# Optimization experiments

Hardware: AMD Instinct MI355X
Metric: run time of the kernel (lower is better)

The kernel has to match this reference:

```python
import jax, jax.numpy as jnp
import numpy as np

N = 50000      # nodes
E = 800000     # edges
F_IN = 128     # n_features
H = 4          # n_heads
C1 = 64        # n_hidden (per-head out of layer 1)
C2 = 32        # n_classes (per-head out of layer 2)
NEG_SLOPE = 0.2
EPS = 1e-16


def setup_inputs() -> dict:
    key = jax.random.key(0)
    ks = jax.random.split(key, 12)
    x = jax.random.normal(ks[0], (N, F_IN), dtype=jnp.float32)
    edge_index = jax.random.randint(ks[1], (2, E), 0, N, dtype=jnp.int64)
    # layer 1 params (GATConv: shared lin for src/dst, att_src/att_dst vectors, bias)
    W1 = jax.random.normal(ks[2], (F_IN, H * C1), dtype=jnp.float32) * (1.0 / np.sqrt(F_IN))
    att_src1 = jax.random.normal(ks[3], (H, C1), dtype=jnp.float32) * 0.1
    att_dst1 = jax.random.normal(ks[4], (H, C1), dtype=jnp.float32) * 0.1
    b1 = jnp.zeros((C1,), dtype=jnp.float32)
    # layer 2 params
    W2 = jax.random.normal(ks[5], (C1, H * C2), dtype=jnp.float32) * (1.0 / np.sqrt(C1))
    att_src2 = jax.random.normal(ks[6], (H, C2), dtype=jnp.float32) * 0.1
    att_dst2 = jax.random.normal(ks[7], (H, C2), dtype=jnp.float32) * 0.1
    b2 = jnp.zeros((C2,), dtype=jnp.float32)
    return {"x": x, "edge_index": edge_index,
            "W1": W1, "att_src1": att_src1, "att_dst1": att_dst1, "b1": b1,
            "W2": W2, "att_src2": att_src2, "att_dst2": att_dst2, "b2": b2}


def gat_conv(x, src, dst, W, att_src, att_dst, b, heads, out_ch):
    """PyG GATConv with concat=False (head-averaged output)."""
    n = x.shape[0]
    h = (x @ W).reshape(n, heads, out_ch)                 # [N, H, C]
    a_s = jnp.einsum('nhc,hc->nh', h, att_src)            # [N, H]
    a_d = jnp.einsum('nhc,hc->nh', h, att_dst)            # [N, H]
    e = jax.nn.leaky_relu(a_s[src] + a_d[dst], NEG_SLOPE)  # [E, H]
    # segment softmax over edges grouped by destination node
    m = jax.ops.segment_max(e, dst, num_segments=n)        # [N, H]
    m = jnp.where(jnp.isfinite(m), m, 0.0)
    ex = jnp.exp(e - m[dst])                               # [E, H]
    denom = jax.ops.segment_sum(ex, dst, num_segments=n)   # [N, H]
    alpha = ex / (denom[dst] + EPS)                        # [E, H]
    # scatter-add aggregation of attended source features
    msg = alpha[:, :, None] * h[src]                       # [E, H, C]
    out = jax.ops.segment_sum(msg, dst, num_segments=n)    # [N, H, C]
    return out.mean(axis=1) + b                            # [N, C]


def reference(x, edge_index, W1, att_src1, att_dst1, b1, W2, att_src2, att_dst2, b2):
    src, dst = edge_index[0], edge_index[1]
    h = jax.nn.relu(gat_conv(x, src, dst, W1, att_src1, att_dst1, b1, H, C1))
    # dropout is identity in eval mode
    out = gat_conv(h, src, dst, W2, att_src2, att_dst2, b2, H, C2)
    return out
```

## Files before the change

kernel.cpp:

```cpp
#include <hip/hip_runtime.h>
#include <hip/hip_fp16.h>
#include <cstdint>
#include <cstddef>

#define N_NODES 50000
#define N_EDGES 800000
#define F_IN 128
#define H_HEADS 4
#define C1 64
#define C2 32
#define NEG_SLOPE 0.2f
#define EPS_GAT 1e-16f
#define SLOT_CAP 96
#define FILL_BPG 256
#define NODES_PER_GROUP 6250
#define GEMM1_BLOCKS 782
#define CBASE ((int)0xAAAAAAAAu)

typedef _Float16 half8 __attribute__((ext_vector_type(8)));
typedef float f32x4 __attribute__((ext_vector_type(4)));

template<int K, int M>
__device__ __forceinline__ void wtrans_dev(const float* __restrict__ W,
                                           _Float16* __restrict__ Wt,
                                           _Float16* tile, int bm, int bk) {
    const int m0 = bm * 64, k0 = bk * 64;
    const int t = threadIdx.x;
    const int c = t & 63;
#pragma unroll
    for (int j = 0; j < 16; ++j) {
        int r = (t >> 6) + 4 * j;
        tile[c * 66 + r] = (_Float16)W[(size_t)(k0 + r) * M + m0 + c];
    }
    __syncthreads();
#pragma unroll
    for (int j = 0; j < 16; ++j) {
        int m_l = (t >> 6) + 4 * j;
        Wt[(size_t)(m0 + m_l) * K + k0 + c] = tile[m_l * 66 + c];
    }
}

__global__ __launch_bounds__(256) void wtrans_kernel(
        const float* __restrict__ W1, _Float16* __restrict__ wt1,
        const float* __restrict__ W2, _Float16* __restrict__ wt2) {
    __shared__ _Float16 tile[64 * 66];
    const int b = blockIdx.x;
    if (b < 8) {
        wtrans_dev<F_IN, H_HEADS * C1>(W1, wt1, tile, b & 3, b >> 2);
    } else {
        wtrans_dev<C1, H_HEADS * C2>(W2, wt2, tile, b - 8, 0);
    }
}

__device__ __forceinline__ void fill_dev(
        const int* __restrict__ src, const int* __restrict__ dst,
        int* __restrict__ cursor, unsigned short* __restrict__ slots,
        int fb) {
    const int g = (fb + (GEMM1_BLOCKS & 7)) & 7;
    const int bg = fb >> 3;
    const int dlo = g * NODES_PER_GROUP;
    const int dhi = dlo + NODES_PER_GROUP;
    const int4* dst4 = (const int4*)dst;
    const int4* src4 = (const int4*)src;
    constexpr int NV4 = N_EDGES / 4;
    for (int v = bg * 256 + (int)threadIdx.x; v < NV4; v += FILL_BPG * 256) {
        int4 d4 = dst4[v];
        int4 s4 = src4[v];
        if (d4.x >= dlo && d4.x < dhi) {
            unsigned int p = (unsigned int)(atomicAdd(&cursor[d4.x], 1) - CBASE);
            if (p < SLOT_CAP) slots[(size_t)d4.x * SLOT_CAP + p] = (unsigned short)s4.x;
        }
        if (d4.y >= dlo && d4.y < dhi) {
            unsigned int p = (unsigned int)(atomicAdd(&cursor[d4.y], 1) - CBASE);
            if (p < SLOT_CAP) slots[(size_t)d4.y * SLOT_CAP + p] = (unsigned short)s4.y;
        }
        if (d4.z >= dlo && d4.z < dhi) {
            unsigned int p = (unsigned int)(atomicAdd(&cursor[d4.z], 1) - CBASE);
            if (p < SLOT_CAP) slots[(size_t)d4.z * SLOT_CAP + p] = (unsigned short)s4.z;
        }
        if (d4.w >= dlo && d4.w < dhi) {
            unsigned int p = (unsigned int)(atomicAdd(&cursor[d4.w], 1) - CBASE);
            if (p < SLOT_CAP) slots[(size_t)d4.w * SLOT_CAP + p] = (unsigned short)s4.w;
        }
    }
}

template<int K, int M, int Hn, int C, typename InT>
__device__ __forceinline__ void gemm_att_dev(
        const InT* __restrict__ X, const _Float16* __restrict__ Wt,
        _Float16* __restrict__ Hout,
        const float* __restrict__ atts, const float* __restrict__ attd,
        float* __restrict__ as_, float* __restrict__ ad_, int Nr,
        _Float16* Ah, _Float16* Bt, _Float16* Ht, int row0) {
    constexpr int LDK = K + 8;
    constexpr int NCT = M / 64;
    constexpr int HPB = 64 / C;
    const int t = threadIdx.x;
    const int wv = t >> 6;
    const int lane = t & 63;
    const int quad = lane >> 4;
    const int n16 = lane & 15;

    if constexpr (sizeof(InT) == 4) {
        constexpr int KQ = K / 4;
#pragma unroll
        for (int j = 0; j < (64 * KQ) / 256; ++j) {
            int flat = t + 256 * j;
            int r = flat / KQ, kq = flat % KQ;
            int rg = row0 + r;
            float4 v = make_float4(0.f, 0.f, 0.f, 0.f);
            if (rg < Nr) v = *(const float4*)&X[(size_t)rg * K + 4 * kq];
            _Float16 tmp[4] = {(_Float16)v.x, (_Float16)v.y, (_Float16)v.z, (_Float16)v.w};
            *(uint2*)&Ah[r * LDK + 4 * kq] = *(const uint2*)tmp;
        }
    } else {
        constexpr int KQ = K / 8;
#pragma unroll
        for (int j = 0; j < (64 * KQ) / 256; ++j) {
            int flat = t + 256 * j;
            int r = flat / KQ, kq = flat % KQ;
            int rg = row0 + r;
            uint4 v = make_uint4(0u, 0u, 0u, 0u);
            if (rg < Nr) v = *(const uint4*)&X[(size_t)rg * K + 8 * kq];
            *(uint4*)&Ah[r * LDK + 8 * kq] = v;
        }
    }
    __syncthreads();

    half8 af[K / 32];
    const _Float16* Ap = &Ah[(16 * wv + n16) * LDK + 8 * quad];
#pragma unroll
    for (int ki = 0; ki < K / 32; ++ki) af[ki] = *(const half8*)(Ap + 32 * ki);

    for (int ct = 0; ct < NCT; ++ct) {
        const int col0 = 64 * ct;
        __syncthreads();
        {
            constexpr int KQ8 = K / 8;
#pragma unroll
            for (int j = 0; j < (64 * KQ8) / 256; ++j) {
                int flat = t + 256 * j;
                int c = flat / KQ8, kq = flat % KQ8;
                uint4 v = *(const uint4*)&Wt[(size_t)(col0 + c) * K + 8 * kq];
                *(uint4*)&Bt[c * LDK + 8 * kq] = v;
            }
        }
        __syncthreads();

        f32x4 acc[4];
#pragma unroll
        for (int nf = 0; nf < 4; ++nf) acc[nf] = (f32x4){0.f, 0.f, 0.f, 0.f};
#pragma unroll
        for (int ki = 0; ki < K / 32; ++ki) {
#pragma unroll
            for (int nf = 0; nf < 4; ++nf) {
                half8 bf = *(const half8*)&Bt[(16 * nf + n16) * LDK + 32 * ki + 8 * quad];
                acc[nf] = __builtin_amdgcn_mfma_f32_16x16x32_f16(af[ki], bf, acc[nf], 0, 0, 0);
            }
        }

        float dps[HPB][4], dpd[HPB][4];
#pragma unroll
        for (int u = 0; u < HPB; ++u)
#pragma unroll
            for (int r = 0; r < 4; ++r) { dps[u][r] = 0.f; dpd[u][r] = 0.f; }
#pragma unroll
        for (int nf = 0; nf < 4; ++nf) {
            int gc = col0 + 16 * nf + n16;
            float cs = atts[gc], cd = attd[gc];
#pragma unroll
            for (int r = 0; r < 4; ++r) {
                float av = acc[nf][r];
                dps[(16 * nf) / C][r] += av * cs;
                dpd[(16 * nf) / C][r] += av * cd;
            }
        }
#pragma unroll
        for (int u = 0; u < HPB; ++u)
#pragma unroll
            for (int r = 0; r < 4; ++r) {
                float s = dps[u][r], d = dpd[u][r];
#pragma unroll
                for (int off = 1; off < 16; off <<= 1) {
                    s += __shfl_xor(s, off, 64);
                    d += __shfl_xor(d, off, 64);
                }
                dps[u][r] = s; dpd[u][r] = d;
            }
        if (n16 == 0) {
            const int h0 = col0 / C;
#pragma unroll
            for (int r = 0; r < 4; ++r) {
                int row = row0 + 16 * wv + 4 * quad + r;
                if (row < Nr) {
#pragma unroll
                    for (int u = 0; u < HPB; ++u) {
                        as_[row * Hn + h0 + u] = dps[u][r];
                        ad_[row * Hn + h0 + u] = dpd[u][r];
                    }
                }
            }
        }

#pragma unroll
        for (int nf = 0; nf < 4; ++nf)
#pragma unroll
            for (int r = 0; r < 4; ++r)
                Ht[(16 * wv + 4 * quad + r) * 72 + 16 * nf + n16] = (_Float16)acc[nf][r];
        __syncthreads();
#pragma unroll
        for (int j = 0; j < 2; ++j) {
            int chunk = t + 256 * j;
            int r = chunk >> 3, cc = chunk & 7;
            int row = row0 + r;
            if (row < Nr) {
                uint4 v = *(const uint4*)&Ht[r * 72 + 8 * cc];
                *(uint4*)&Hout[(size_t)row * M + col0 + 8 * cc] = v;
            }
        }
    }
}

__global__ __launch_bounds__(256) void gemm1_fill_kernel(
        const float* __restrict__ x, const _Float16* __restrict__ wt1,
        _Float16* __restrict__ h1,
        const float* __restrict__ atts, const float* __restrict__ attd,
        float* __restrict__ as_, float* __restrict__ ad_,
        const int* __restrict__ src, const int* __restrict__ dst,
        int* __restrict__ cursor, unsigned short* __restrict__ slots) {
    constexpr int LDK = F_IN + 8;
    __shared__ _Float16 Ah[64 * LDK];
    __shared__ _Float16 Bt[64 * LDK];
    __shared__ _Float16 Ht[64 * 72];
    if (blockIdx.x < GEMM1_BLOCKS) {
        gemm_att_dev<F_IN, H_HEADS * C1, H_HEADS, C1, float>(
            x, wt1, h1, atts, attd, as_, ad_, N_NODES,
            Ah, Bt, Ht, blockIdx.x * 64);
    } else {
        fill_dev(src, dst, cursor, slots, blockIdx.x - GEMM1_BLOCKS);
    }
}

__global__ __launch_bounds__(256) void agg1_mv_kernel(
        const int* __restrict__ degp, const unsigned short* __restrict__ slots,
        const float* __restrict__ as_, const float* __restrict__ ad_,
        const _Float16* __restrict__ Hm, const float* __restrict__ bias,
        const _Float16* __restrict__ wt2,
        const float* __restrict__ atts2, const float* __restrict__ attd2,
        _Float16* __restrict__ h2, float* __restrict__ as2_,
        float* __restrict__ ad2_, int Nr) {
    constexpr int Hn = H_HEADS;
    constexpr int HC = Hn * C1;
    constexpr int PER = 16;
    int node = blockIdx.x * 4 + (threadIdx.x >> 6);
    int lane = threadIdx.x & 63;
    if (node >= Nr) return;
    const int g = lane >> 4;
    const int l = lane & 15;
    const int h = l >> 2;
    const float ad_h = ad_[node * Hn + h];

    const int dn = min(degp[node] - CBASE, SLOT_CAP);
    const int begin = node * SLOT_CAP;
    const int end = begin + dn;
    const int iters = (dn + 3) >> 2;

    float acc[PER];
#pragma unroll
    for (int t = 0; t < PER; ++t) acc[t] = 0.f;
    float wsum = 0.f;

    int idx = begin + g;
    bool okA = idx < end;
    int sA = (int)slots[okA ? idx : begin];
    float aA = as_[sA * Hn + h];
    uint4 uA[2];
    {
        const uint4* hp = (const uint4*)(Hm + (size_t)sA * HC + l * PER);
        uA[0] = hp[0]; uA[1] = hp[1];
    }

#pragma unroll 2
    for (int it = 0; it < iters; ++it) {
        const int j = idx + 4;
        const bool okB = j < end;
        int sB = (int)slots[okB ? j : begin];
        float aB = as_[sB * Hn + h];
        uint4 uB[2];
        {
            const uint4* hp = (const uint4*)(Hm + (size_t)sB * HC + l * PER);
            uB[0] = hp[0]; uB[1] = hp[1];
        }

        float logit = aA + ad_h;
        float lr = fmaxf(logit, NEG_SLOPE * logit);
        float w = okA ? __expf(lr) : 0.f;
        wsum += w;
#pragma unroll
        for (int v = 0; v < 2; ++v) {
            half8 hv = __builtin_bit_cast(half8, uA[v]);
#pragma unroll
            for (int e = 0; e < 8; ++e)
                acc[8 * v + e] = fmaf((float)hv[e], w, acc[8 * v + e]);
        }
        okA = okB; aA = aB; uA[0] = uB[0]; uA[1] = uB[1];
        idx = j;
    }

#pragma unroll
    for (int t = 0; t < PER; ++t) {
        acc[t] += __shfl_xor(acc[t], 16, 64);
        acc[t] += __shfl_xor(acc[t], 32, 64);
    }
    wsum += __shfl_xor(wsum, 16, 64);
    wsum += __shfl_xor(wsum, 32, 64);
    const float inv = 1.f / (wsum + EPS_GAT);
    const int q = lane & 3;
    float val[PER];
#pragma unroll
    for (int t = 0; t < PER; ++t) {
        float v = acc[t] * inv;
        v += __shfl_xor(v, 4, 64);
        v += __shfl_xor(v, 8, 64);
        v = v * (1.0f / Hn) + bias[q * PER + t];
        val[t] = fmaxf(v, 0.f);
    }

    const int r = lane >> 2;
    float p[8];
#pragma unroll
    for (int k = 0; k < 8; ++k) {
        const _Float16* wrow = wt2 + (size_t)(r + 16 * k) * C1 + q * PER;
        half8 wa = *(const half8*)wrow;
        half8 wb = *(const half8*)(wrow + 8);
        float s = 0.f;
#pragma unroll
        for (int e = 0; e < 8; ++e) s = fmaf((float)wa[e], val[e], s);
#pragma unroll
        for (int e = 0; e < 8; ++e) s = fmaf((float)wb[e], val[8 + e], s);
        p[k] = s;
    }
#pragma unroll
    for (int k = 0; k < 8; ++k) {
        p[k] += __shfl_xor(p[k], 1, 64);
        p[k] += __shfl_xor(p[k], 2, 64);
    }

    float asum[4], adsum[4];
#pragma unroll
    for (int hh = 0; hh < 4; ++hh) {
        int m0 = r + 32 * hh, m1 = m0 + 16;
        float a = p[2 * hh] * atts2[m0] + p[2 * hh + 1] * atts2[m1];
        float d = p[2 * hh] * attd2[m0] + p[2 * hh + 1] * attd2[m1];
        asum[hh] = (q == 0) ? a : 0.f;
        adsum[hh] = (q == 0) ? d : 0.f;
    }
#pragma unroll
    for (int hh = 0; hh < 4; ++hh) {
#pragma unroll
        for (int off = 1; off < 64; off <<= 1) {
            asum[hh] += __shfl_xor(asum[hh], off, 64);
            adsum[hh] += __shfl_xor(adsum[hh], off, 64);
        }
    }
    if (lane == 0) {
#pragma unroll
        for (int hh = 0; hh < 4; ++hh) {
            as2_[node * Hn + hh] = asum[hh];
            ad2_[node * Hn + hh] = adsum[hh];
        }
    }

    if (q == 0) {
        _Float16* hp = h2 + (size_t)node * (H_HEADS * C2);
#pragma unroll
        for (int k = 0; k < 8; ++k) hp[r + 16 * k] = (_Float16)p[k];
    }
}

template<int Hn, int C, bool RELU, bool OUT_F16>
__global__ __launch_bounds__(256) void gat_agg_kernel(
        const int* __restrict__ degp, const unsigned short* __restrict__ slots,
        const float* __restrict__ as_, const float* __restrict__ ad_,
        const _Float16* __restrict__ Hm, const float* __restrict__ bias,
        void* __restrict__ outv, int Nr) {
    constexpr int HC = Hn * C;
    constexpr int PER = HC / 16;
    constexpr int NV = PER / 8;
    int node = blockIdx.x * 4 + (threadIdx.x >> 6);
    int lane = threadIdx.x & 63;
    if (node >= Nr) return;
    const int g = lane >> 4;
    const int l = lane & 15;
    const int h = l >> 2;
    const float ad_h = ad_[node * Hn + h];

    const int dn = min(degp[node] - CBASE, SLOT_CAP);
    const int begin = node * SLOT_CAP;
    const int end = begin + dn;
    const int iters = (dn + 3) >> 2;

    float acc[PER];
#pragma unroll
    for (int t = 0; t < PER; ++t) acc[t] = 0.f;
    float wsum = 0.f;

    int idx = begin + g;
    bool okA = idx < end;
    int sA = (int)slots[okA ? idx : begin];
    float aA = as_[sA * Hn + h];
    uint4 uA[NV];
    {
        const uint4* hp = (const uint4*)(Hm + (size_t)sA * HC + l * PER);
        uA[0] = hp[0];
        if constexpr (NV == 2) uA[1] = hp[1];
    }

#pragma unroll 2
    for (int it = 0; it < iters; ++it) {
        const int j = idx + 4;
        const bool okB = j < end;
        int sB = (int)slots[okB ? j : begin];
        float aB = as_[sB * Hn + h];
        uint4 uB[NV];
        {
            const uint4* hp = (const uint4*)(Hm + (size_t)sB * HC + l * PER);
            uB[0] = hp[0];
            if constexpr (NV == 2) uB[1] = hp[1];
        }

        float logit = aA + ad_h;
        float lr = fmaxf(logit, NEG_SLOPE * logit);
        float w = okA ? __expf(lr) : 0.f;
        wsum += w;
#pragma unroll
        for (int v = 0; v < NV; ++v) {
            half8 hv = __builtin_bit_cast(half8, uA[v]);
#pragma unroll
            for (int e = 0; e < 8; ++e)
                acc[8 * v + e] = fmaf((float)hv[e], w, acc[8 * v + e]);
        }
        okA = okB; aA = aB;
        uA[0] = uB[0];
        if constexpr (NV == 2) uA[1] = uB[1];
        idx = j;
    }

#pragma unroll
    for (int t = 0; t < PER; ++t) {
        acc[t] += __shfl_xor(acc[t], 16, 64);
        acc[t] += __shfl_xor(acc[t], 32, 64);
    }
    wsum += __shfl_xor(wsum, 16, 64);
    wsum += __shfl_xor(wsum, 32, 64);
    const float inv = 1.f / (wsum + EPS_GAT);
    float val[PER];
#pragma unroll
    for (int t = 0; t < PER; ++t) {
        float v = acc[t] * inv;
        v += __shfl_xor(v, 4, 64);
        v += __shfl_xor(v, 8, 64);
        val[t] = v * (1.0f / Hn);
    }
    if (lane < 4) {
        const int c0 = lane * PER;
#pragma unroll
        for (int t = 0; t < PER; ++t) {
            float v = val[t] + bias[c0 + t];
            if (RELU) v = fmaxf(v, 0.f);
            val[t] = v;
        }
        if constexpr (OUT_F16) {
            _Float16* o = (_Float16*)outv;
            _Float16 tmp[PER];
#pragma unroll
            for (int t = 0; t < PER; ++t) tmp[t] = (_Float16)val[t];
            uint4* d4 = (uint4*)&o[(size_t)node * C + c0];
            d4[0] = *(const uint4*)&tmp[0];
            if constexpr (NV == 2) d4[1] = *(const uint4*)&tmp[8];
        } else {
            float* o = (float*)outv;
#pragma unroll
            for (int t4 = 0; t4 < PER / 4; ++t4)
                *(float4*)&o[(size_t)node * C + c0 + 4 * t4] =
                    make_float4(val[4 * t4 + 0], val[4 * t4 + 1],
                                val[4 * t4 + 2], val[4 * t4 + 3]);
        }
    }
}

extern "C" void kernel_launch(void* const* d_in, const int* in_sizes, int n_in,
                              void* d_out, int out_size, void* d_ws, size_t ws_size,
                              hipStream_t stream) {
    const float* x    = (const float*)d_in[0];
    const int*   ei   = (const int*)d_in[1];
    const float* W1   = (const float*)d_in[2];
    const float* as1w = (const float*)d_in[3];
    const float* ad1w = (const float*)d_in[4];
    const float* b1   = (const float*)d_in[5];
    const float* W2   = (const float*)d_in[6];
    const float* as2w = (const float*)d_in[7];
    const float* ad2w = (const float*)d_in[8];
    const float* b2   = (const float*)d_in[9];
    float* out = (float*)d_out;

    const int* src = ei;
    const int* dst = ei + N_EDGES;

    char* ws = (char*)d_ws;
    size_t off = 0;
    auto alloc = [&](size_t bytes) -> void* {
        void* p = ws + off;
        off = (off + bytes + 255) & ~(size_t)255;
        return p;
    };
    int*   cursor = (int*)alloc((size_t)N_NODES * 4);
    float* as1_ = (float*)alloc((size_t)N_NODES * H_HEADS * 4);
    float* ad1_ = (float*)alloc((size_t)N_NODES * H_HEADS * 4);
    float* as2_ = (float*)alloc((size_t)N_NODES * H_HEADS * 4);
    float* ad2_ = (float*)alloc((size_t)N_NODES * H_HEADS * 4);
    _Float16* h1   = (_Float16*)alloc((size_t)N_NODES * H_HEADS * C1 * 2);
    _Float16* h2   = (_Float16*)alloc((size_t)N_NODES * H_HEADS * C2 * 2);
    _Float16* wt1  = (_Float16*)alloc((size_t)(H_HEADS * C1) * F_IN * 2);
    _Float16* wt2  = (_Float16*)alloc((size_t)(H_HEADS * C2) * C1 * 2);
    unsigned short* slots = (unsigned short*)alloc((size_t)N_NODES * SLOT_CAP * 2);

    wtrans_kernel<<<10, 256, 0, stream>>>(W1, wt1, W2, wt2);

    gemm1_fill_kernel<<<GEMM1_BLOCKS + 8 * FILL_BPG, 256, 0, stream>>>(
        x, wt1, h1, as1w, ad1w, as1_, ad1_, src, dst, cursor, slots);

    agg1_mv_kernel<<<(N_NODES + 3) / 4, 256, 0, stream>>>(
        cursor, slots, as1_, ad1_, h1, b1, wt2, as2w, ad2w,
        h2, as2_, ad2_, N_NODES);

    gat_agg_kernel<H_HEADS, C2, false, false><<<(N_NODES + 3) / 4, 256, 0, stream>>>(
        cursor, slots, as2_, ad2_, h2, b2, (void*)out, N_NODES);
}
```

Baseline: 262.4 us.

## Reorder layer-2 linear transform after aggregation and fold attention vectors into W2

Attention logits for layer 2 are now computed from the 64-wide layer-1 output through precomputed vectors W2·att, which an extra wtrans block builds. Layer 1 no longer runs the per-node GEMV. The second aggregation gathers the 64-wide fp16 out1 rows instead of the 128-wide h2 rows and applies W2 per head after the weighted sum, using shared memory and a small matvec per node. This halves the per-edge gather bytes in layer 2 and removes the mid-pipeline GEMV, in exchange for a per-node GEMV after aggregation and some shared-memory traffic.

Measured after the change: 337.4 us. 28.6% more time.

```diff
diff --git a/kernel.cpp b/kernel.cpp
--- a/kernel.cpp
+++ b/kernel.cpp
@@ -18,6 +18,7 @@
 #define CBASE ((int)0xAAAAAAAAu)
 
 typedef _Float16 half8 __attribute__((ext_vector_type(8)));
+typedef _Float16 half4 __attribute__((ext_vector_type(4)));
 typedef float f32x4 __attribute__((ext_vector_type(4)));
 
 template<int K, int M>
@@ -42,13 +43,27 @@
 
 __global__ __launch_bounds__(256) void wtrans_kernel(
         const float* __restrict__ W1, _Float16* __restrict__ wt1,
-        const float* __restrict__ W2, _Float16* __restrict__ wt2) {
+        const float* __restrict__ W2, _Float16* __restrict__ wt2,
+        const float* __restrict__ as2w, const float* __restrict__ ad2w,
+        float* __restrict__ vs2, float* __restrict__ vd2) {
     __shared__ _Float16 tile[64 * 66];
     const int b = blockIdx.x;
     if (b < 8) {
         wtrans_dev<F_IN, H_HEADS * C1>(W1, wt1, tile, b & 3, b >> 2);
+    } else if (b < 10) {
+        wtrans_dev<C1, H_HEADS * C2>(W2, wt2, tile, b - 8, 0);
     } else {
-        wtrans_dev<C1, H_HEADS * C2>(W2, wt2, tile, b - 8, 0);
+        const int t = threadIdx.x;
+        const int h = t >> 6, c = t & 63;
+        float s = 0.f, d = 0.f;
+#pragma unroll
+        for (int c2 = 0; c2 < C2; ++c2) {
+            float w = W2[(size_t)c * (H_HEADS * C2) + h * C2 + c2];
+            s = fmaf(w, as2w[h * C2 + c2], s);
+            d = fmaf(w, ad2w[h * C2 + c2], d);
+        }
+        vs2[h * 64 + c] = s;
+        vd2[h * 64 + c] = d;
     }
 }
 
@@ -241,20 +256,18 @@
     }
 }
 
-__global__ __launch_bounds__(256) void agg1_mv_kernel(
+__global__ __launch_bounds__(256) void agg1_kernel(
         const int* __restrict__ degp, const unsigned short* __restrict__ slots,
         const float* __restrict__ as_, const float* __restrict__ ad_,
         const _Float16* __restrict__ Hm, const float* __restrict__ bias,
-        const _Float16* __restrict__ wt2,
-        const float* __restrict__ atts2, const float* __restrict__ attd2,
-        _Float16* __restrict__ h2, float* __restrict__ as2_,
-        float* __restrict__ ad2_, int Nr) {
+        _Float16* __restrict__ out1,
+        const float* __restrict__ vs2, const float* __restrict__ vd2,
+        float* __restrict__ as2_, float* __restrict__ ad2_) {
     constexpr int Hn = H_HEADS;
     constexpr int HC = Hn * C1;
     constexpr int PER = 16;
     int node = blockIdx.x * 4 + (threadIdx.x >> 6);
     int lane = threadIdx.x & 63;
-    if (node >= Nr) return;
     const int g = lane >> 4;
     const int l = lane & 15;
     const int h = l >> 2;
@@ -315,177 +328,176 @@
     wsum += __shfl_xor(wsum, 16, 64);
     wsum += __shfl_xor(wsum, 32, 64);
     const float inv = 1.f / (wsum + EPS_GAT);
-    const int q = lane & 3;
     float val[PER];
 #pragma unroll
     for (int t = 0; t < PER; ++t) {
         float v = acc[t] * inv;
         v += __shfl_xor(v, 4, 64);
         v += __shfl_xor(v, 8, 64);
-        v = v * (1.0f / Hn) + bias[q * PER + t];
-        val[t] = fmaxf(v, 0.f);
-    }
-
-    const int r = lane >> 2;
-    float p[8];
-#pragma unroll
-    for (int k = 0; k < 8; ++k) {
-        const _Float16* wrow = wt2 + (size_t)(r + 16 * k) * C1 + q * PER;
-        half8 wa = *(const half8*)wrow;
-        half8 wb = *(const half8*)(wrow + 8);
-        float s = 0.f;
-#pragma unroll
-        for (int e = 0; e < 8; ++e) s = fmaf((float)wa[e], val[e], s);
-#pragma unroll
-        for (int e = 0; e < 8; ++e) s = fmaf((float)wb[e], val[8 + e], s);
-        p[k] = s;
-    }
-#pragma unroll
-    for (int k = 0; k < 8; ++k) {
-        p[k] += __shfl_xor(p[k], 1, 64);
-        p[k] += __shfl_xor(p[k], 2, 64);
-    }
-
-    float asum[4], adsum[4];
-#pragma unroll
-    for (int hh = 0; hh < 4; ++hh) {
-        int m0 = r + 32 * hh, m1 = m0 + 16;
-        float a = p[2 * hh] * atts2[m0] + p[2 * hh + 1] * atts2[m1];
-        float d = p[2 * hh] * attd2[m0] + p[2 * hh + 1] * attd2[m1];
-        asum[hh] = (q == 0) ? a : 0.f;
-        adsum[hh] = (q == 0) ? d : 0.f;
-    }
-#pragma unroll
-    for (int hh = 0; hh < 4; ++hh) {
-#pragma unroll
-        for (int off = 1; off < 64; off <<= 1) {
-            asum[hh] += __shfl_xor(asum[hh], off, 64);
-            adsum[hh] += __shfl_xor(adsum[hh], off, 64);
-        }
-    }
-    if (lane == 0) {
+        val[t] = v * (1.0f / Hn);
+    }
+    if (lane < 4) {
+        const int c0 = lane * PER;
+#pragma unroll
+        for (int t = 0; t < PER; ++t)
+            val[t] = fmaxf(val[t] + bias[c0 + t], 0.f);
+
+        _Float16 tmp[PER];
+#pragma unroll
+        for (int t = 0; t < PER; ++t) tmp[t] = (_Float16)val[t];
+        uint4* d4 = (uint4*)&out1[(size_t)node * C1 + c0];
+        d4[0] = *(const uint4*)&tmp[0];
+        d4[1] = *(const uint4*)&tmp[8];
+
+        float ps[4] = {0.f, 0.f, 0.f, 0.f}, pd[4] = {0.f, 0.f, 0.f, 0.f};
 #pragma unroll
         for (int hh = 0; hh < 4; ++hh) {
-            as2_[node * Hn + hh] = asum[hh];
-            ad2_[node * Hn + hh] = adsum[hh];
-        }
-    }
-
-    if (q == 0) {
-        _Float16* hp = h2 + (size_t)node * (H_HEADS * C2);
-#pragma unroll
-        for (int k = 0; k < 8; ++k) hp[r + 16 * k] = (_Float16)p[k];
-    }
-}
-
-template<int Hn, int C, bool RELU, bool OUT_F16>
-__global__ __launch_bounds__(256) void gat_agg_kernel(
+            const float4* vsp = (const float4*)&vs2[hh * 64 + c0];
+            const float4* vdp = (const float4*)&vd2[hh * 64 + c0];
+#pragma unroll
+            for (int t4 = 0; t4 < 4; ++t4) {
+                float4 a = vsp[t4], b = vdp[t4];
+                ps[hh] = fmaf(val[4 * t4 + 0], a.x, ps[hh]);
+                ps[hh] = fmaf(val[4 * t4 + 1], a.y, ps[hh]);
+                ps[hh] = fmaf(val[4 * t4 + 2], a.z, ps[hh]);
+                ps[hh] = fmaf(val[4 * t4 + 3], a.w, ps[hh]);
+                pd[hh] = fmaf(val[4 * t4 + 0], b.x, pd[hh]);
+                pd[hh] = fmaf(val[4 * t4 + 1], b.y, pd[hh]);
+                pd[hh] = fmaf(val[4 * t4 + 2], b.z, pd[hh]);
+                pd[hh] = fmaf(val[4 * t4 + 3], b.w, pd[hh]);
+            }
+        }
+#pragma unroll
+        for (int hh = 0; hh < 4; ++hh) {
+            ps[hh] += __shfl_xor(ps[hh], 1, 64);
+            ps[hh] += __shfl_xor(ps[hh], 2, 64);
+            pd[hh] += __shfl_xor(pd[hh], 1, 64);
+            pd[hh] += __shfl_xor(pd[hh], 2, 64);
+        }
+        if (lane == 0) {
+            *(float4*)&as2_[node * 4] = make_float4(ps[0], ps[1], ps[2], ps[3]);
+            *(float4*)&ad2_[node * 4] = make_float4(pd[0], pd[1], pd[2], pd[3]);
+        }
+    }
+}
+
+__global__ __launch_bounds__(256) void agg2_kernel(
         const int* __restrict__ degp, const unsigned short* __restrict__ slots,
-        const float* __restrict__ as_, const float* __restrict__ ad_,
-        const _Float16* __restrict__ Hm, const float* __restrict__ bias,
-        void* __restrict__ outv, int Nr) {
-    constexpr int HC = Hn * C;
-    constexpr int PER = HC / 16;
-    constexpr int NV = PER / 8;
-    int node = blockIdx.x * 4 + (threadIdx.x >> 6);
-    int lane = threadIdx.x & 63;
-    if (node >= Nr) return;
+        const float* __restrict__ as2_, const float* __restrict__ ad2_,
+        const _Float16* __restrict__ out1, const float* __restrict__ b2,
+        const _Float16* __restrict__ wt2, float* __restrict__ out) {
+    __shared__ float aggL[4][4][64];
+    const int wv = threadIdx.x >> 6;
+    const int node = blockIdx.x * 4 + wv;
+    const int lane = threadIdx.x & 63;
     const int g = lane >> 4;
     const int l = lane & 15;
-    const int h = l >> 2;
-    const float ad_h = ad_[node * Hn + h];
-
+
+    float adh[4];
+    {
+        float4 t = *(const float4*)&ad2_[node * 4];
+        adh[0] = t.x; adh[1] = t.y; adh[2] = t.z; adh[3] = t.w;
+    }
     const int dn = min(degp[node] - CBASE, SLOT_CAP);
     const int begin = node * SLOT_CAP;
     const int end = begin + dn;
     const int iters = (dn + 3) >> 2;
 
-    float acc[PER];
-#pragma unroll
-    for (int t = 0; t < PER; ++t) acc[t] = 0.f;
-    float wsum = 0.f;
+    float acc[4][4];
+#pragma unroll
+    for (int hh = 0; hh < 4; ++hh)
+#pragma unroll
+        for (int j = 0; j < 4; ++j) acc[hh][j] = 0.f;
+    float wsum[4] = {0.f, 0.f, 0.f, 0.f};
 
     int idx = begin + g;
     bool okA = idx < end;
     int sA = (int)slots[okA ? idx : begin];
-    float aA = as_[sA * Hn + h];
-    uint4 uA[NV];
-    {
-        const uint4* hp = (const uint4*)(Hm + (size_t)sA * HC + l * PER);
-        uA[0] = hp[0];
-        if constexpr (NV == 2) uA[1] = hp[1];
-    }
+    float4 aA = *(const float4*)&as2_[sA * 4];
+    uint2 uA = *(const uint2*)(out1 + (size_t)sA * C1 + l * 4);
 
 #pragma unroll 2
     for (int it = 0; it < iters; ++it) {
         const int j = idx + 4;
         const bool okB = j < end;
         int sB = (int)slots[okB ? j : begin];
-        float aB = as_[sB * Hn + h];
-        uint4 uB[NV];
+        float4 aB = *(const float4*)&as2_[sB * 4];
+        uint2 uB = *(const uint2*)(out1 + (size_t)sB * C1 + l * 4);
+
+        float w[4];
         {
-            const uint4* hp = (const uint4*)(Hm + (size_t)sB * HC + l * PER);
-            uB[0] = hp[0];
-            if constexpr (NV == 2) uB[1] = hp[1];
-        }
-
-        float logit = aA + ad_h;
-        float lr = fmaxf(logit, NEG_SLOPE * logit);
-        float w = okA ? __expf(lr) : 0.f;
-        wsum += w;
-#pragma unroll
-        for (int v = 0; v < NV; ++v) {
-            half8 hv = __builtin_bit_cast(half8, uA[v]);
-#pragma unroll
-            for (int e = 0; e < 8; ++e)
-                acc[8 * v + e] = fmaf((float)hv[e], w, acc[8 * v + e]);
-        }
-        okA = okB; aA = aB;
-        uA[0] = uB[0];
-        if constexpr (NV == 2) uA[1] = uB[1];
+            float lg0 = aA.x + adh[0], lg1 = aA.y + adh[1];
+            float lg2 = aA.z + adh[2], lg3 = aA.w + adh[3];
+            lg0 = fmaxf(lg0, NEG_SLOPE * lg0);
+            lg1 = fmaxf(lg1, NEG_SLOPE * lg1);
+            lg2 = fmaxf(lg2, NEG_SLOPE * lg2);
+            lg3 = fmaxf(lg3, NEG_SLOPE * lg3);
+            w[0] = okA ? __expf(lg0) : 0.f;
+            w[1] = okA ? __expf(lg1) : 0.f;
+            w[2] = okA ? __expf(lg2) : 0.f;
+            w[3] = okA ? __expf(lg3) : 0.f;
+        }
+#pragma unroll
+        for (int hh = 0; hh < 4; ++hh) wsum[hh] += w[hh];
+        half4 hv = __builtin_bit_cast(half4, uA);
+#pragma unroll
+        for (int hh = 0; hh < 4; ++hh)
+#pragma unroll
+            for (int e = 0; e < 4; ++e)
+                acc[hh][e] = fmaf((float)hv[e], w[hh], acc[hh][e]);
+
+        okA = okB; aA = aB; uA = uB;
         idx = j;
     }
 
 #pragma unroll
-    for (int t = 0; t < PER; ++t) {
-        acc[t] += __shfl_xor(acc[t], 16, 64);
-        acc[t] += __shfl_xor(acc[t], 32, 64);
-    }
-    wsum += __shfl_xor(wsum, 16, 64);
-    wsum += __shfl_xor(wsum, 32, 64);
-    const float inv = 1.f / (wsum + EPS_GAT);
-    float val[PER];
-#pragma unroll
-    for (int t = 0; t < PER; ++t) {
-        float v = acc[t] * inv;
-        v += __shfl_xor(v, 4, 64);
-        v += __shfl_xor(v, 8, 64);
-        val[t] = v * (1.0f / Hn);
-    }
-    if (lane < 4) {
-        const int c0 = lane * PER;
-#pragma unroll
-        for (int t = 0; t < PER; ++t) {
-            float v = val[t] + bias[c0 + t];
-            if (RELU) v = fmaxf(v, 0.f);
-            val[t] = v;
-        }
-        if constexpr (OUT_F16) {
-            _Float16* o = (_Float16*)outv;
-            _Float16 tmp[PER];
-#pragma unroll
-            for (int t = 0; t < PER; ++t) tmp[t] = (_Float16)val[t];
-            uint4* d4 = (uint4*)&o[(size_t)node * C + c0];
-            d4[0] = *(const uint4*)&tmp[0];
-            if constexpr (NV == 2) d4[1] = *(const uint4*)&tmp[8];
-        } else {
-            float* o = (float*)outv;
-#pragma unroll
-            for (int t4 = 0; t4 < PER / 4; ++t4)
-                *(float4*)&o[(size_t)node * C + c0 + 4 * t4] =
-                    make_float4(val[4 * t4 + 0], val[4 * t4 + 1],
-                                val[4 * t4 + 2], val[4 * t4 + 3]);
-        }
+    for (int hh = 0; hh < 4; ++hh) {
+#pragma unroll
+        for (int e = 0; e < 4; ++e) {
+            acc[hh][e] += __shfl_xor(acc[hh][e], 16, 64);
+            acc[hh][e] += __shfl_xor(acc[hh][e], 32, 64);
+        }
+        wsum[hh] += __shfl_xor(wsum[hh], 16, 64);
+        wsum[hh] += __shfl_xor(wsum[hh], 32, 64);
+    }
+#pragma unroll
+    for (int hh = 0; hh < 4; ++hh) {
+        float inv = 1.f / (wsum[hh] + EPS_GAT);
+#pragma unroll
+        for (int e = 0; e < 4; ++e) acc[hh][e] *= inv;
+    }
+
+    if (lane < 16) {
+#pragma unroll
+        for (int hh = 0; hh < 4; ++hh)
+            *(float4*)&aggL[wv][hh][l * 4] =
+                make_float4(acc[hh][0], acc[hh][1], acc[hh][2], acc[hh][3]);
+    }
+
+    const int hh = lane >> 4;
+    const int c2 = lane & 15;
+    const float* arow = aggL[wv][hh];
+    const _Float16* w0 = wt2 + (size_t)(hh * C2 + c2) * C1;
+    const _Float16* w1 = wt2 + (size_t)(hh * C2 + c2 + 16) * C1;
+    float y0 = 0.f, y1 = 0.f;
+#pragma unroll
+    for (int cb = 0; cb < 8; ++cb) {
+        half8 wa = *(const half8*)(w0 + cb * 8);
+        half8 wb = *(const half8*)(w1 + cb * 8);
+#pragma unroll
+        for (int e = 0; e < 8; ++e) {
+            float a = arow[cb * 8 + e];
+            y0 = fmaf((float)wa[e], a, y0);
+            y1 = fmaf((float)wb[e], a, y1);
+        }
+    }
+    y0 += __shfl_xor(y0, 16, 64);
+    y0 += __shfl_xor(y0, 32, 64);
+    y1 += __shfl_xor(y1, 16, 64);
+    y1 += __shfl_xor(y1, 32, 64);
+    if (lane < 16) {
+        out[(size_t)node * C2 + c2]      = 0.25f * y0 + b2[c2];
+        out[(size_t)node * C2 + c2 + 16] = 0.25f * y1 + b2[c2 + 16];
     }
 }
 
@@ -520,20 +532,21 @@
     float* as2_ = (float*)alloc((size_t)N_NODES * H_HEADS * 4);
     float* ad2_ = (float*)alloc((size_t)N_NODES * H_HEADS * 4);
     _Float16* h1   = (_Float16*)alloc((size_t)N_NODES * H_HEADS * C1 * 2);
-    _Float16* h2   = (_Float16*)alloc((size_t)N_NODES * H_HEADS * C2 * 2);
+    _Float16* out1 = (_Float16*)alloc((size_t)N_NODES * C1 * 2);
     _Float16* wt1  = (_Float16*)alloc((size_t)(H_HEADS * C1) * F_IN * 2);
     _Float16* wt2  = (_Float16*)alloc((size_t)(H_HEADS * C2) * C1 * 2);
+    float* vs2 = (float*)alloc((size_t)H_HEADS * C1 * 4);
+    float* vd2 = (float*)alloc((size_t)H_HEADS * C1 * 4);
     unsigned short* slots = (unsigned short*)alloc((size_t)N_NODES * SLOT_CAP * 2);
 
-    wtrans_kernel<<<10, 256, 0, stream>>>(W1, wt1, W2, wt2);
+    wtrans_kernel<<<11, 256, 0, stream>>>(W1, wt1, W2, wt2, as2w, ad2w, vs2, vd2);
 
     gemm1_fill_kernel<<<GEMM1_BLOCKS + 8 * FILL_BPG, 256, 0, stream>>>(
         x, wt1, h1, as1w, ad1w, as1_, ad1_, src, dst, cursor, slots);
 
-    agg1_mv_kernel<<<(N_NODES + 3) / 4, 256, 0, stream>>>(
-        cursor, slots, as1_, ad1_, h1, b1, wt2, as2w, ad2w,
-        h2, as2_, ad2_, N_NODES);
-
-    gat_agg_kernel<H_HEADS, C2, false, false><<<(N_NODES + 3) / 4, 256, 0, stream>>>(
-        cursor, slots, as2_, ad2_, h2, b2, (void*)out, N_NODES);
-}
+    agg1_kernel<<<(N_NODES + 3) / 4, 256, 0, stream>>>(
+        cursor, slots, as1_, ad1_, h1, b1, out1, vs2, vd2, as2_, ad2_);
+
+    agg2_kernel<<<(N_NODES + 3) / 4, 256, 0, stream>>>(
+        cursor, slots, as2_, ad2_, out1, b2, wt2, out);
+}
```
